# Kernel optimization log

Measured on AMD Instinct MI355X. Metric: run time of the kernel, lower is better.

## Reference

```python
import jax, jax.numpy as jnp
import numpy as np

B, N, C = 16, 2048, 3           # images, proposals/image, classes (incl. background)
K = 100                         # num_detections kept per class
SCORE_THRESH = 0.05
NMS_THRESH = 0.5
MIN_ANGLE = 10.0                # process_box min width (self.min_angle)
WX, WW = 1.0, 1.0               # box_coder reg_weights
NEG = jnp.float32(-1e9)


def setup_inputs() -> dict:
    key = jax.random.key(0)
    k1, k2, k3, k4 = jax.random.split(key, 4)
    class_logit = jax.random.normal(k1, (B, N, C), jnp.float32)
    box_regression = jax.random.normal(k2, (B, N, 2 * C), jnp.float32) * 0.1
    starts = jax.random.uniform(k3, (B, N), dtype=jnp.float32) * 300.0
    widths = jax.random.uniform(k4, (B, N), dtype=jnp.float32) * 50.0 + 12.0
    proposal = jnp.stack([starts, starts + widths], axis=-1)  # [B,N,2] 1-D intervals
    return {"class_logit": class_logit, "box_regression": box_regression,
            "proposal": proposal, "image_shape": 360}


def _decode(delta, prop):
    w = prop[:, 1] - prop[:, 0]
    ctr = prop[:, 0] + 0.5 * w
    dx = delta[:, 0] / WX
    dw = jnp.minimum(delta[:, 1] / WW, 4.0)  # clamp like torchvision
    pc = dx * w + ctr
    pw = jnp.exp(dw) * w
    return jnp.stack([pc - 0.5 * pw, pc + 0.5 * pw], axis=-1)  # [N,2]


def _iou_1d(a, b):
    inter = jnp.maximum(0.0, jnp.minimum(a[:, None, 1], b[None, :, 1])
                        - jnp.maximum(a[:, None, 0], b[None, :, 0]))
    union = (a[:, None, 1] - a[:, None, 0]) + (b[None, :, 1] - b[None, :, 0]) - inter
    return inter / jnp.maximum(union, 1e-8)  # [Na,Nb]


def _infer_one_class(score, delta, prop, image_shape):
    # score [N], delta [N,2], prop [N,2] -> [K,3] (start, end, score); invalid slots score=NEG
    box = _decode(delta, prop)
    lo = jnp.clip(box[:, 0], 0.0, image_shape)
    hi = jnp.clip(box[:, 1], 0.0, image_shape)
    box = jnp.stack([lo, hi], axis=-1)
    valid = ((hi - lo) >= MIN_ANGLE) & (score >= SCORE_THRESH)
    ms = jnp.where(valid, score, NEG)
    order = jnp.argsort(-ms)
    b = box[order]
    s = ms[order]
    sup = jax.lax.stop_gradient(_iou_1d(b, b)) > NMS_THRESH  # [N,N] bool
    idx = jnp.arange(N)

    def body(keep, i):  # greedy NMS in score order
        kill = sup[i] & keep[i] & (idx > i)
        return keep & ~kill, None

    keep0 = s > 0.5 * NEG
    keep, _ = jax.lax.scan(body, keep0, idx)
    ks = jnp.where(keep, s, NEG)
    top_s, top_i = jax.lax.top_k(ks, K)
    top_b = b[top_i]
    return jnp.concatenate([top_b, top_s[:, None]], axis=-1)  # [K,3]


def reference(class_logit, box_regression, proposal, image_shape):
    img = jnp.float32(image_shape)
    scores = jax.nn.softmax(class_logit, axis=-1)[..., 1:]        # [B,N,C-1] fg classes
    deltas = box_regression.reshape(B, N, C, 2)[:, :, 1:]         # [B,N,C-1,2]
    scores = jnp.moveaxis(scores, -1, 1)                          # [B,C-1,N]
    deltas = jnp.moveaxis(deltas, 2, 1)                           # [B,C-1,N,2]
    f = jax.vmap(jax.vmap(_infer_one_class, in_axes=(0, 0, None, None)),
                 in_axes=(0, 0, 0, None))
    return f(scores, deltas, proposal, img)  # [B, C-1, K, 3]
```

## Files before the change

kernel.cpp:

```cpp
#include <hip/hip_runtime.h>
#include <math.h>

#define B_IMG 16
#define N_PROP 2048
#define C_CLS 3
#define K_OUT 100
#define NTHREADS 1024
#define NWAVES (NTHREADS / 64)
#define NBLK64 (N_PROP / 64)
#define NUNITS (B_IMG * N_PROP)

__device__ __forceinline__ unsigned long long shfl_xor_u64(unsigned long long v, int lx) {
    unsigned int lo = (unsigned int)__shfl_xor((int)(unsigned int)(v & 0xffffffffull), lx, 64);
    unsigned int hi = (unsigned int)__shfl_xor((int)(unsigned int)(v >> 32), lx, 64);
    return ((unsigned long long)hi << 32) | (unsigned long long)lo;
}
__device__ __forceinline__ float readlane_f(float v, int l) {
    return __int_as_float(__builtin_amdgcn_readlane(__float_as_int(v), l));
}
__device__ __forceinline__ bool iou_gt_half(float inter, float uni) {
    double b = (double)fmaxf(uni, 1e-8f);
    return (double)inter * 2.0 > b * 0x1.000001p0;
}
__device__ __forceinline__ float parse_imgf(int raw) {
    return (raw > 0 && raw < 1000000) ? (float)raw : __int_as_float(raw);
}

__global__ __launch_bounds__(256)
void decode_kernel(const float* __restrict__ class_logit,
                   const float* __restrict__ box_reg,
                   const float* __restrict__ proposal,
                   const int* __restrict__ image_shape_p,
                   unsigned long long* __restrict__ wskey,
                   float2* __restrict__ wbox)
{
#pragma clang fp contract(off)
    const int t = blockIdx.x * 256 + threadIdx.x;
    const int n = t & (N_PROP - 1);
    const float imgf = parse_imgf(image_shape_p[0]);

    const float* lg = class_logit + (size_t)t * C_CLS;
    float l0 = lg[0], l1 = lg[1], l2 = lg[2];
    float mx = fmaxf(l0, fmaxf(l1, l2));
    float e0 = (float)exp((double)(l0 - mx));
    float e1 = (float)exp((double)(l1 - mx));
    float e2 = (float)exp((double)(l2 - mx));
    float denom = (e0 + e1) + e2;

    const float* pp = proposal + (size_t)t * 2;
    float pA = pp[0], pB = pp[1];
    float w = pB - pA;
    float ctr = pA + 0.5f * w;

    const float* dr = box_reg + (size_t)t * (2 * C_CLS);
    float d1x = dr[2], d1w = dr[3], d2x = dr[4], d2w = dr[5];

#pragma unroll
    for (int c = 0; c < 2; ++c) {
        float score = ((c == 0) ? e1 : e2) / denom;
        float dx = (c == 0) ? d1x : d2x;
        float dw = fminf((c == 0) ? d1w : d2w, 4.0f);
        float tt = dx * w;
        float pc = tt + ctr;
        float pw = (float)exp((double)dw) * w;
        float half = 0.5f * pw;
        float lo = pc - half;
        float hi = pc + half;
        lo = fminf(fmaxf(lo, 0.0f), imgf);
        hi = fminf(fmaxf(hi, 0.0f), imgf);
        bool valid = ((hi - lo) >= 10.0f) && (score >= 0.05f);
        float ms = valid ? score : -1e9f;
        unsigned int u = __float_as_uint(ms);
        unsigned int e = (u & 0x80000000u) ? ~u : (u | 0x80000000u);
        wskey[c * NUNITS + t] = ((unsigned long long)e << 32) |
                                (unsigned long long)(0xFFFFFFFFu - (unsigned int)n);
        wbox[c * NUNITS + t] = make_float2(lo, hi);
    }
}

__global__ __launch_bounds__(NTHREADS)
void roiheads_kernel(const unsigned long long* __restrict__ wskey,
                     const float2* __restrict__ wbox,
                     float* __restrict__ out)
{
#pragma clang fp contract(off)
    __shared__ unsigned long long skey[N_PROP];
    __shared__ float slo[N_PROP], shi[N_PROP];
    __shared__ unsigned char keep[N_PROP];
    __shared__ unsigned short alv[2][N_PROP];
    __shared__ float clo[64], chi[64];
    __shared__ unsigned long long kmask[NBLK64];
    __shared__ int wsum[NWAVES];
    __shared__ int sh_nvalid, sh_ccnt;

    const int tid = threadIdx.x;
    const int lane = tid & 63;
    const int wid = tid >> 6;
    const int img = blockIdx.x >> 1;
    const int cls = blockIdx.x & 1;
    const size_t base = (size_t)cls * NUNITS + (size_t)img * N_PROP;

    if (tid == 0) sh_nvalid = 0;

    const int p0 = (wid << 7) | (lane << 1);
    const int p1 = p0 | 1;

    unsigned long long r0 = wskey[base + p0];
    unsigned long long r1 = wskey[base + p1];

    auto pass_inreg = [&](int k, int j) {
        if (j == 1) {
            bool desc = ((p0 & k) == 0);
            bool sw = desc ? (r0 < r1) : (r0 > r1);
            if (sw) { unsigned long long t = r0; r0 = r1; r1 = t; }
        } else {
            int lx = j >> 1;
            unsigned long long o0 = shfl_xor_u64(r0, lx);
            unsigned long long o1 = shfl_xor_u64(r1, lx);
            bool desc = ((p0 & k) == 0);
            bool lower = ((p0 & j) == 0);
            bool takeMax = (lower == desc);
            r0 = takeMax ? (r0 > o0 ? r0 : o0) : (r0 < o0 ? r0 : o0);
            r1 = takeMax ? (r1 > o1 ? r1 : o1) : (r1 < o1 ? r1 : o1);
        }
    };

    for (int k = 2; k <= 128; k <<= 1)
        for (int j = k >> 1; j >= 1; j >>= 1)
            pass_inreg(k, j);

    for (int k = 256; k <= N_PROP; k <<= 1) {
        skey[p0] = r0; skey[p1] = r1;
        __syncthreads();
        for (int j = k >> 1; j >= 128; j >>= 1) {
            int i = ((tid & ~(j - 1)) << 1) | (tid & (j - 1));
            int part = i | j;
            unsigned long long a = skey[i], b = skey[part];
            bool desc_blk = ((i & k) == 0);
            bool sw = desc_blk ? (a < b) : (a > b);
            if (sw) { skey[i] = b; skey[part] = a; }
            __syncthreads();
        }
        r0 = skey[p0]; r1 = skey[p1];
        for (int j = 64; j >= 1; j >>= 1)
            pass_inreg(k, j);
    }
    skey[p0] = r0; skey[p1] = r1;
    __syncthreads();

    for (int i = tid; i < N_PROP; i += NTHREADS) {
        unsigned long long kk = skey[i];
        unsigned int e = (unsigned int)(kk >> 32);
        unsigned int sb = (e & 0x80000000u) ? (e & 0x7FFFFFFFu) : ~e;
        float s = __uint_as_float(sb);
        unsigned int n = 0xFFFFFFFFu - (unsigned int)(kk & 0xFFFFFFFFull);
        float2 bx = wbox[base + n];
        slo[i] = bx.x;
        shi[i] = bx.y;
        keep[i] = 0;
        bool v = (s > -5e8f);
        unsigned long long mb = __ballot(v);
        if (lane == 0) atomicAdd(&sh_nvalid, __popcll(mb));
        alv[0][i] = (unsigned short)i;
    }
    __syncthreads();

    int na = sh_nvalid;
    int cur = 0;
    int tk = 0;
    const unsigned long long below = (1ull << lane) - 1ull;

    while (na > 0) {
        const int m = (na < 64) ? na : 64;
        if (tid < 64) {
            bool inr = (lane < m);
            unsigned short p = inr ? alv[cur][lane] : (unsigned short)0;
            float blo = inr ? slo[p] : 0.0f;
            float bhi = inr ? shi[p] : 0.0f;
            float bw = bhi - blo;
            unsigned long long A = (m >= 64) ? ~0ull : ((1ull << m) - 1ull);
            unsigned long long kept = 0;
            while (A) {
                int c = __builtin_ctzll(A);
                float cl = readlane_f(blo, c);
                float ch = readlane_f(bhi, c);
                float inter = fmaxf(fminf(bhi, ch) - fmaxf(blo, cl), 0.0f);
                float uni = bw + (ch - cl) - inter;
                bool kill = (lane > c) && iou_gt_half(inter, uni);
                unsigned long long row = __ballot(kill);
                kept |= (1ull << c);
                A &= ~(row | (1ull << c));
            }
            bool alive = inr && ((kept >> lane) & 1ull);
            if (alive) keep[p] = 1;
            int rank = __popcll(kept & below);
            if (alive) { clo[rank] = blo; chi[rank] = bhi; }
            if (lane == 0) sh_ccnt = __popcll(kept);
        }
        __syncthreads();
        const int cnt = sh_ccnt;
        tk += cnt;
        if (tk >= K_OUT) break;

        float klo = 0.0f, khi = 0.0f;
        if (lane < cnt) { klo = clo[lane]; khi = chi[lane]; }
        int base2 = 0;
        for (int start = 64; start < na; start += NTHREADS) {
            int t = start + tid;
            unsigned short q = 0;
            bool surv = false;
            if (t < na) {
                q = alv[cur][t];
                float qlo = slo[q], qhi = shi[q];
                float qw = qhi - qlo;
                bool dead = false;
                for (int r = 0; r < cnt; ++r) {
                    float cl = readlane_f(klo, r);
                    float ch = readlane_f(khi, r);
                    float inter = fmaxf(fminf(qhi, ch) - fmaxf(qlo, cl), 0.0f);
                    float uni = qw + (ch - cl) - inter;
                    dead |= iou_gt_half(inter, uni);
                }
                surv = !dead;
            }
            unsigned long long mb = __ballot(surv);
            if (lane == 0) wsum[wid] = __popcll(mb);
            __syncthreads();
            int off = base2, tot = base2;
            for (int w2 = 0; w2 < NWAVES; ++w2) {
                int c2 = wsum[w2];
                if (w2 < wid) off += c2;
                tot += c2;
            }
            if (surv) alv[cur ^ 1][off + __popcll(mb & below)] = q;
            base2 = tot;
            __syncthreads();
        }
        na = base2;
        cur ^= 1;
    }

    for (int blk = wid; blk < NBLK64; blk += NWAVES) {
        bool kk = keep[blk * 64 + lane] != 0;
        unsigned long long mb = __ballot(kk);
        if (lane == 0) kmask[blk] = mb;
    }
    __syncthreads();
    {
        float* outp = out + (((size_t)img * 2 + cls) * K_OUT) * 3;
        for (int blk = wid; blk < NBLK64; blk += NWAVES) {
            int kc = 0, nc = 0, nk = 0;
            for (int b = 0; b < NBLK64; ++b) {
                int pc = __popcll(kmask[b]);
                nk += pc;
                if (b < blk) { kc += pc; nc += 64 - pc; }
            }
            if (kc >= K_OUT && nk + nc >= K_OUT && nc >= K_OUT) continue;
            int p = blk * 64 + lane;
            unsigned long long mb = kmask[blk];
            bool k = (mb >> lane) & 1ull;
            int rk = kc + __popcll(mb & below);
            int rn = nc + __popcll((~mb) & below);
            if (k) {
                if (rk < K_OUT) {
                    unsigned long long kk2 = skey[p];
                    unsigned int e = (unsigned int)(kk2 >> 32);
                    unsigned int sb = (e & 0x80000000u) ? (e & 0x7FFFFFFFu) : ~e;
                    outp[rk * 3 + 0] = slo[p];
                    outp[rk * 3 + 1] = shi[p];
                    outp[rk * 3 + 2] = __uint_as_float(sb);
                }
            } else {
                int oi = nk + rn;
                if (oi < K_OUT) {
                    outp[oi * 3 + 0] = slo[p];
                    outp[oi * 3 + 1] = shi[p];
                    outp[oi * 3 + 2] = -1e9f;
                }
            }
        }
    }
}

extern "C" void kernel_launch(void* const* d_in, const int* in_sizes, int n_in,
                              void* d_out, int out_size, void* d_ws, size_t ws_size,
                              hipStream_t stream) {
    const float* class_logit = (const float*)d_in[0];
    const float* box_reg     = (const float*)d_in[1];
    const float* prop        = (const float*)d_in[2];
    const int*   image_shape = (const int*)d_in[3];
    float* out = (float*)d_out;

    unsigned long long* wskey = (unsigned long long*)d_ws;
    float2* wbox = (float2*)((char*)d_ws + 2 * NUNITS * sizeof(unsigned long long));

    decode_kernel<<<dim3(NUNITS / 256), dim3(256), 0, stream>>>(
        class_logit, box_reg, prop, image_shape, wskey, wbox);
    roiheads_kernel<<<dim3(B_IMG * 2), dim3(NTHREADS), 0, stream>>>(
        wskey, wbox, out);
}
```

Baseline: 99.51 us.

## Preselect top candidates via histogram and sort only a 512-element subset

Builds a 4096-bin histogram of the top key bits to find a threshold admitting at least 256 top-scoring proposals. It compacts and bitonic-sorts only up to 512 of them, then runs greedy NMS on that subset. If the subset yields fewer than K kept boxes, it falls back to a full 2048-element sort and NMS. The block size drops from 1024 to 256 threads, which reduces sort cost but makes the fallback path and NMS compaction loops slower.

```diff
diff --git a/kernel.cpp b/kernel.cpp
--- a/kernel.cpp
+++ b/kernel.cpp
@@ -5,10 +5,13 @@
 #define N_PROP 2048
 #define C_CLS 3
 #define K_OUT 100
-#define NTHREADS 1024
-#define NWAVES (NTHREADS / 64)
+#define NUNITS (B_IMG * N_PROP)
+
+#define NTH2 256
+#define NW2 (NTH2 / 64)
 #define NBLK64 (N_PROP / 64)
-#define NUNITS (B_IMG * N_PROP)
+#define SORTN 512
+#define TSEL 256
 
 __device__ __forceinline__ unsigned long long shfl_xor_u64(unsigned long long v, int lx) {
     unsigned int lo = (unsigned int)__shfl_xor((int)(unsigned int)(v & 0xffffffffull), lx, 64);
@@ -17,6 +20,9 @@
 }
 __device__ __forceinline__ float readlane_f(float v, int l) {
     return __int_as_float(__builtin_amdgcn_readlane(__float_as_int(v), l));
+}
+__device__ __forceinline__ unsigned int readlane_u32(unsigned int v, int l) {
+    return (unsigned int)__builtin_amdgcn_readlane((int)v, l);
 }
 __device__ __forceinline__ bool iou_gt_half(float inter, float uni) {
     double b = (double)fmaxf(uni, 1e-8f);
@@ -78,20 +84,21 @@
     }
 }
 
-__global__ __launch_bounds__(NTHREADS)
-void roiheads_kernel(const unsigned long long* __restrict__ wskey,
-                     const float2* __restrict__ wbox,
-                     float* __restrict__ out)
+__global__ __launch_bounds__(NTH2)
+void nms_kernel(const unsigned long long* __restrict__ wskey,
+                const float2* __restrict__ wbox,
+                float* __restrict__ out)
 {
 #pragma clang fp contract(off)
     __shared__ unsigned long long skey[N_PROP];
     __shared__ float slo[N_PROP], shi[N_PROP];
     __shared__ unsigned char keep[N_PROP];
     __shared__ unsigned short alv[2][N_PROP];
+    __shared__ unsigned int hist[4096];
     __shared__ float clo[64], chi[64];
     __shared__ unsigned long long kmask[NBLK64];
-    __shared__ int wsum[NWAVES];
-    __shared__ int sh_nvalid, sh_ccnt;
+    __shared__ int wsum[NW2];
+    __shared__ int sh_cnt, sh_nv, sh_ccnt, sh_thr, sh_M;
 
     const int tid = threadIdx.x;
     const int lane = tid & 63;
@@ -99,163 +106,139 @@
     const int img = blockIdx.x >> 1;
     const int cls = blockIdx.x & 1;
     const size_t base = (size_t)cls * NUNITS + (size_t)img * N_PROP;
-
-    if (tid == 0) sh_nvalid = 0;
-
-    const int p0 = (wid << 7) | (lane << 1);
-    const int p1 = p0 | 1;
-
-    unsigned long long r0 = wskey[base + p0];
-    unsigned long long r1 = wskey[base + p1];
-
-    auto pass_inreg = [&](int k, int j) {
-        if (j == 1) {
-            bool desc = ((p0 & k) == 0);
-            bool sw = desc ? (r0 < r1) : (r0 > r1);
-            if (sw) { unsigned long long t = r0; r0 = r1; r1 = t; }
-        } else {
-            int lx = j >> 1;
-            unsigned long long o0 = shfl_xor_u64(r0, lx);
-            unsigned long long o1 = shfl_xor_u64(r1, lx);
-            bool desc = ((p0 & k) == 0);
-            bool lower = ((p0 & j) == 0);
-            bool takeMax = (lower == desc);
-            r0 = takeMax ? (r0 > o0 ? r0 : o0) : (r0 < o0 ? r0 : o0);
-            r1 = takeMax ? (r1 > o1 ? r1 : o1) : (r1 < o1 ? r1 : o1);
-        }
+    const unsigned long long below = (1ull << lane) - 1ull;
+
+    for (int i = tid; i < 4096; i += NTH2) hist[i] = 0;
+    if (tid == 0) { sh_cnt = 0; }
+    __syncthreads();
+
+    unsigned long long k8[8];
+#pragma unroll
+    for (int u = 0; u < 8; ++u) {
+        unsigned long long k = wskey[base + u * NTH2 + tid];
+        k8[u] = k;
+        atomicAdd(&hist[(unsigned int)(k >> 52)], 1u);
+    }
+    __syncthreads();
+
+    if (wid == 0) {
+        unsigned int csum = 0;
+        int b0 = lane * 64;
+        for (int i = 0; i < 64; ++i) csum += hist[b0 + i];
+        unsigned int S = csum;
+        for (int d = 1; d < 64; d <<= 1) {
+            unsigned int t2 = __shfl_down(S, d, 64);
+            if (lane + d < 64) S += t2;
+        }
+        unsigned long long bm = __ballot(S >= (unsigned)TSEL);
+        int lstar = 63 - __clzll((long long)bm);
+        unsigned int Snext = 0;
+        if (lstar < 63) Snext = readlane_u32(S, lstar + 1);
+        if (lane == 0) {
+            unsigned int G = Snext;
+            int b = lstar * 64 + 63;
+            for (; b >= lstar * 64; --b) {
+                G += hist[b];
+                if (G >= (unsigned)TSEL) break;
+            }
+            sh_thr = b; sh_M = (int)G;
+        }
+    }
+    __syncthreads();
+    const unsigned int thr = (unsigned int)sh_thr;
+    const int M = sh_M;
+
+    auto run_nms = [&](int total) -> int {
+#pragma clang fp contract(off)
+        int na = sh_nv;
+        int cur = 0, tk = 0;
+        while (na > 0) {
+            const int m = (na < 64) ? na : 64;
+            if (tid < 64) {
+                bool inr = (lane < m);
+                unsigned short p = inr ? alv[cur][lane] : (unsigned short)0;
+                float blo = inr ? slo[p] : 0.0f;
+                float bhi = inr ? shi[p] : 0.0f;
+                float bw = bhi - blo;
+                unsigned long long A = (m >= 64) ? ~0ull : ((1ull << m) - 1ull);
+                unsigned long long kept = 0;
+                while (A) {
+                    int c = __builtin_ctzll(A);
+                    float cl = readlane_f(blo, c);
+                    float ch = readlane_f(bhi, c);
+                    float inter = fmaxf(fminf(bhi, ch) - fmaxf(blo, cl), 0.0f);
+                    float uni = bw + (ch - cl) - inter;
+                    bool kill = (lane > c) && iou_gt_half(inter, uni);
+                    unsigned long long row = __ballot(kill);
+                    kept |= (1ull << c);
+                    A &= ~(row | (1ull << c));
+                }
+                bool alive = inr && ((kept >> lane) & 1ull);
+                if (alive) keep[p] = 1;
+                int rank = __popcll(kept & below);
+                if (alive) { clo[rank] = blo; chi[rank] = bhi; }
+                if (lane == 0) sh_ccnt = __popcll(kept);
+            }
+            __syncthreads();
+            const int cnt = sh_ccnt;
+            tk += cnt;
+            if (tk >= K_OUT) break;
+
+            float klo = 0.0f, khi = 0.0f;
+            if (lane < cnt) { klo = clo[lane]; khi = chi[lane]; }
+            int base2 = 0;
+            for (int start = 64; start < na; start += NTH2) {
+                int t2 = start + tid;
+                unsigned short q = 0;
+                bool surv = false;
+                if (t2 < na) {
+                    q = alv[cur][t2];
+                    float qlo = slo[q], qhi = shi[q];
+                    float qw = qhi - qlo;
+                    bool dead = false;
+                    for (int r = 0; r < cnt; ++r) {
+                        float cl = readlane_f(klo, r);
+                        float ch = readlane_f(khi, r);
+                        float inter = fmaxf(fminf(qhi, ch) - fmaxf(qlo, cl), 0.0f);
+                        float uni = qw + (ch - cl) - inter;
+                        dead |= iou_gt_half(inter, uni);
+                    }
+                    surv = !dead;
+                }
+                unsigned long long mb = __ballot(surv);
+                if (lane == 0) wsum[wid] = __popcll(mb);
+                __syncthreads();
+                int off = base2, tot = base2;
+                for (int w2 = 0; w2 < NW2; ++w2) {
+                    int c2 = wsum[w2];
+                    if (w2 < wid) off += c2;
+                    tot += c2;
+                }
+                if (surv) alv[cur ^ 1][off + __popcll(mb & below)] = q;
+                base2 = tot;
+                __syncthreads();
+            }
+            na = base2;
+            cur ^= 1;
+        }
+        return tk;
     };
 
-    for (int k = 2; k <= 128; k <<= 1)
-        for (int j = k >> 1; j >= 1; j >>= 1)
-            pass_inreg(k, j);
-
-    for (int k = 256; k <= N_PROP; k <<= 1) {
-        skey[p0] = r0; skey[p1] = r1;
-        __syncthreads();
-        for (int j = k >> 1; j >= 128; j >>= 1) {
-            int i = ((tid & ~(j - 1)) << 1) | (tid & (j - 1));
-            int part = i | j;
-            unsigned long long a = skey[i], b = skey[part];
-            bool desc_blk = ((i & k) == 0);
-            bool sw = desc_blk ? (a < b) : (a > b);
-            if (sw) { skey[i] = b; skey[part] = a; }
-            __syncthreads();
-        }
-        r0 = skey[p0]; r1 = skey[p1];
-        for (int j = 64; j >= 1; j >>= 1)
-            pass_inreg(k, j);
-    }
-    skey[p0] = r0; skey[p1] = r1;
-    __syncthreads();
-
-    for (int i = tid; i < N_PROP; i += NTHREADS) {
-        unsigned long long kk = skey[i];
-        unsigned int e = (unsigned int)(kk >> 32);
-        unsigned int sb = (e & 0x80000000u) ? (e & 0x7FFFFFFFu) : ~e;
-        float s = __uint_as_float(sb);
-        unsigned int n = 0xFFFFFFFFu - (unsigned int)(kk & 0xFFFFFFFFull);
-        float2 bx = wbox[base + n];
-        slo[i] = bx.x;
-        shi[i] = bx.y;
-        keep[i] = 0;
-        bool v = (s > -5e8f);
-        unsigned long long mb = __ballot(v);
-        if (lane == 0) atomicAdd(&sh_nvalid, __popcll(mb));
-        alv[0][i] = (unsigned short)i;
-    }
-    __syncthreads();
-
-    int na = sh_nvalid;
-    int cur = 0;
-    int tk = 0;
-    const unsigned long long below = (1ull << lane) - 1ull;
-
-    while (na > 0) {
-        const int m = (na < 64) ? na : 64;
-        if (tid < 64) {
-            bool inr = (lane < m);
-            unsigned short p = inr ? alv[cur][lane] : (unsigned short)0;
-            float blo = inr ? slo[p] : 0.0f;
-            float bhi = inr ? shi[p] : 0.0f;
-            float bw = bhi - blo;
-            unsigned long long A = (m >= 64) ? ~0ull : ((1ull << m) - 1ull);
-            unsigned long long kept = 0;
-            while (A) {
-                int c = __builtin_ctzll(A);
-                float cl = readlane_f(blo, c);
-                float ch = readlane_f(bhi, c);
-                float inter = fmaxf(fminf(bhi, ch) - fmaxf(blo, cl), 0.0f);
-                float uni = bw + (ch - cl) - inter;
-                bool kill = (lane > c) && iou_gt_half(inter, uni);
-                unsigned long long row = __ballot(kill);
-                kept |= (1ull << c);
-                A &= ~(row | (1ull << c));
-            }
-            bool alive = inr && ((kept >> lane) & 1ull);
-            if (alive) keep[p] = 1;
-            int rank = __popcll(kept & below);
-            if (alive) { clo[rank] = blo; chi[rank] = bhi; }
-            if (lane == 0) sh_ccnt = __popcll(kept);
-        }
-        __syncthreads();
-        const int cnt = sh_ccnt;
-        tk += cnt;
-        if (tk >= K_OUT) break;
-
-        float klo = 0.0f, khi = 0.0f;
-        if (lane < cnt) { klo = clo[lane]; khi = chi[lane]; }
-        int base2 = 0;
-        for (int start = 64; start < na; start += NTHREADS) {
-            int t = start + tid;
-            unsigned short q = 0;
-            bool surv = false;
-            if (t < na) {
-                q = alv[cur][t];
-                float qlo = slo[q], qhi = shi[q];
-                float qw = qhi - qlo;
-                bool dead = false;
-                for (int r = 0; r < cnt; ++r) {
-                    float cl = readlane_f(klo, r);
-                    float ch = readlane_f(khi, r);
-                    float inter = fmaxf(fminf(qhi, ch) - fmaxf(qlo, cl), 0.0f);
-                    float uni = qw + (ch - cl) - inter;
-                    dead |= iou_gt_half(inter, uni);
-                }
-                surv = !dead;
-            }
-            unsigned long long mb = __ballot(surv);
-            if (lane == 0) wsum[wid] = __popcll(mb);
-            __syncthreads();
-            int off = base2, tot = base2;
-            for (int w2 = 0; w2 < NWAVES; ++w2) {
-                int c2 = wsum[w2];
-                if (w2 < wid) off += c2;
-                tot += c2;
-            }
-            if (surv) alv[cur ^ 1][off + __popcll(mb & below)] = q;
-            base2 = tot;
-            __syncthreads();
-        }
-        na = base2;
-        cur ^= 1;
-    }
-
-    for (int blk = wid; blk < NBLK64; blk += NWAVES) {
-        bool kk = keep[blk * 64 + lane] != 0;
-        unsigned long long mb = __ballot(kk);
-        if (lane == 0) kmask[blk] = mb;
-    }
-    __syncthreads();
-    {
+    auto emit = [&](int nblk) {
+        for (int blk = wid; blk < nblk; blk += NW2) {
+            bool kk = keep[blk * 64 + lane] != 0;
+            unsigned long long mb = __ballot(kk);
+            if (lane == 0) kmask[blk] = mb;
+        }
+        __syncthreads();
         float* outp = out + (((size_t)img * 2 + cls) * K_OUT) * 3;
-        for (int blk = wid; blk < NBLK64; blk += NWAVES) {
+        for (int blk = wid; blk < nblk; blk += NW2) {
             int kc = 0, nc = 0, nk = 0;
-            for (int b = 0; b < NBLK64; ++b) {
+            for (int b = 0; b < nblk; ++b) {
                 int pc = __popcll(kmask[b]);
                 nk += pc;
                 if (b < blk) { kc += pc; nc += 64 - pc; }
             }
-            if (kc >= K_OUT && nk + nc >= K_OUT && nc >= K_OUT) continue;
             int p = blk * 64 + lane;
             unsigned long long mb = kmask[blk];
             bool k = (mb >> lane) & 1ull;
@@ -279,6 +262,120 @@
                 }
             }
         }
+    };
+
+    bool done = false;
+    if (M <= SORTN) {
+        int myc = 0;
+#pragma unroll
+        for (int u = 0; u < 8; ++u) myc += ((unsigned int)(k8[u] >> 52) >= thr);
+        int off = atomicAdd(&sh_cnt, myc);
+#pragma unroll
+        for (int u = 0; u < 8; ++u)
+            if ((unsigned int)(k8[u] >> 52) >= thr) skey[off++] = k8[u];
+        for (int i = M + tid; i < SORTN; i += NTH2) skey[i] = 0ull;
+        __syncthreads();
+
+        const int p0 = (wid << 7) | (lane << 1);
+        const int p1 = p0 | 1;
+        unsigned long long r0 = skey[p0], r1 = skey[p1];
+        auto pass_inreg = [&](int k, int j) {
+            if (j == 1) {
+                bool desc = ((p0 & k) == 0);
+                bool sw = desc ? (r0 < r1) : (r0 > r1);
+                if (sw) { unsigned long long t2 = r0; r0 = r1; r1 = t2; }
+            } else {
+                int lx = j >> 1;
+                unsigned long long o0 = shfl_xor_u64(r0, lx);
+                unsigned long long o1 = shfl_xor_u64(r1, lx);
+                bool desc = ((p0 & k) == 0);
+                bool lower = ((p0 & j) == 0);
+                bool takeMax = (lower == desc);
+                r0 = takeMax ? (r0 > o0 ? r0 : o0) : (r0 < o0 ? r0 : o0);
+                r1 = takeMax ? (r1 > o1 ? r1 : o1) : (r1 < o1 ? r1 : o1);
+            }
+        };
+        for (int k = 2; k <= 128; k <<= 1)
+            for (int j = k >> 1; j >= 1; j >>= 1)
+                pass_inreg(k, j);
+        for (int k = 256; k <= SORTN; k <<= 1) {
+            skey[p0] = r0; skey[p1] = r1;
+            __syncthreads();
+            for (int j = k >> 1; j >= 128; j >>= 1) {
+                int i = ((tid & ~(j - 1)) << 1) | (tid & (j - 1));
+                int part = i | j;
+                unsigned long long a = skey[i], b = skey[part];
+                bool desc_blk = ((i & k) == 0);
+                bool sw = desc_blk ? (a < b) : (a > b);
+                if (sw) { skey[i] = b; skey[part] = a; }
+                __syncthreads();
+            }
+            r0 = skey[p0]; r1 = skey[p1];
+            for (int j = 64; j >= 1; j >>= 1)
+                pass_inreg(k, j);
+        }
+        skey[p0] = r0; skey[p1] = r1;
+        if (tid == 0) sh_nv = 0;
+        __syncthreads();
+
+        for (int i = tid; i < SORTN; i += NTH2) {
+            unsigned long long kk = skey[i];
+            unsigned int e = (unsigned int)(kk >> 32);
+            unsigned int sb = (e & 0x80000000u) ? (e & 0x7FFFFFFFu) : ~e;
+            float s = __uint_as_float(sb);
+            bool inw = (i < M);
+            if (inw) {
+                unsigned int n = 0xFFFFFFFFu - (unsigned int)(kk & 0xFFFFFFFFull);
+                float2 bx = wbox[base + n];
+                slo[i] = bx.x; shi[i] = bx.y;
+            } else { slo[i] = 0.0f; shi[i] = 0.0f; }
+            keep[i] = 0;
+            bool v = inw && (s > -5e8f);
+            unsigned long long mb = __ballot(v);
+            if (lane == 0) atomicAdd(&sh_nv, __popcll(mb));
+            alv[0][i] = (unsigned short)i;
+        }
+        __syncthreads();
+
+        int tk = run_nms(SORTN);
+        if (tk >= K_OUT) { emit(SORTN / 64); done = true; }
+    }
+
+    if (!done) {
+        __syncthreads();
+        for (int i = tid; i < N_PROP; i += NTH2) skey[i] = wskey[base + i];
+        if (tid == 0) sh_nv = 0;
+        __syncthreads();
+        for (int k = 2; k <= N_PROP; k <<= 1) {
+            for (int j = k >> 1; j >= 1; j >>= 1) {
+                for (int s = tid; s < N_PROP / 2; s += NTH2) {
+                    int i = ((s & ~(j - 1)) << 1) | (s & (j - 1));
+                    int part = i | j;
+                    unsigned long long a = skey[i], b = skey[part];
+                    bool desc_blk = ((i & k) == 0);
+                    bool sw = desc_blk ? (a < b) : (a > b);
+                    if (sw) { skey[i] = b; skey[part] = a; }
+                }
+                __syncthreads();
+            }
+        }
+        for (int i = tid; i < N_PROP; i += NTH2) {
+            unsigned long long kk = skey[i];
+            unsigned int e = (unsigned int)(kk >> 32);
+            unsigned int sb = (e & 0x80000000u) ? (e & 0x7FFFFFFFu) : ~e;
+            float s = __uint_as_float(sb);
+            unsigned int n = 0xFFFFFFFFu - (unsigned int)(kk & 0xFFFFFFFFull);
+            float2 bx = wbox[base + n];
+            slo[i] = bx.x; shi[i] = bx.y;
+            keep[i] = 0;
+            bool v = (s > -5e8f);
+            unsigned long long mb = __ballot(v);
+            if (lane == 0) atomicAdd(&sh_nv, __popcll(mb));
+            alv[0][i] = (unsigned short)i;
+        }
+        __syncthreads();
+        (void)run_nms(N_PROP);
+        emit(NBLK64);
     }
 }
 
@@ -296,6 +393,5 @@
 
     decode_kernel<<<dim3(NUNITS / 256), dim3(256), 0, stream>>>(
         class_logit, box_reg, prop, image_shape, wskey, wbox);
-    roiheads_kernel<<<dim3(B_IMG * 2), dim3(NTHREADS), 0, stream>>>(
-        wskey, wbox, out);
-}
+    nms_kernel<<<dim3(B_IMG * 2), dim3(NTH2), 0, stream>>>(wskey, wbox, out);
+}
```

After: 159.3 us. +60.1%, slower.

## Build 64x64 suppression matrix across all waves, resolve greedy chain via readlane

Applied to the files above, without the earlier changes.

Replaces the single-wave serial NMS over each 64-candidate chunk with a parallel step. All 16 waves compute rows of a 64x64 IoU suppression bitmask into shared memory, then every wave redundantly resolves the greedy keep chain with scalar readlanes of the bitmask rows. This takes the IoU arithmetic out of the serial dependency chain, at the cost of an extra barrier and redundant chain resolution in every wave.

```diff
diff --git a/kernel.cpp b/kernel.cpp
--- a/kernel.cpp
+++ b/kernel.cpp
@@ -17,6 +17,11 @@
 }
 __device__ __forceinline__ float readlane_f(float v, int l) {
     return __int_as_float(__builtin_amdgcn_readlane(__float_as_int(v), l));
+}
+__device__ __forceinline__ unsigned long long readlane_u64(unsigned long long v, int l) {
+    unsigned int lo = (unsigned int)__builtin_amdgcn_readlane((int)(unsigned int)(v & 0xffffffffull), l);
+    unsigned int hi = (unsigned int)__builtin_amdgcn_readlane((int)(unsigned int)(v >> 32), l);
+    return ((unsigned long long)hi << 32) | (unsigned long long)lo;
 }
 __device__ __forceinline__ bool iou_gt_half(float inter, float uni) {
     double b = (double)fmaxf(uni, 1e-8f);
@@ -89,9 +94,10 @@
     __shared__ unsigned char keep[N_PROP];
     __shared__ unsigned short alv[2][N_PROP];
     __shared__ float clo[64], chi[64];
+    __shared__ unsigned long long sup[64];
     __shared__ unsigned long long kmask[NBLK64];
     __shared__ int wsum[NWAVES];
-    __shared__ int sh_nvalid, sh_ccnt;
+    __shared__ int sh_nvalid;
 
     const int tid = threadIdx.x;
     const int lane = tid & 63;
@@ -172,33 +178,47 @@
 
     while (na > 0) {
         const int m = (na < 64) ? na : 64;
-        if (tid < 64) {
-            bool inr = (lane < m);
-            unsigned short p = inr ? alv[cur][lane] : (unsigned short)0;
-            float blo = inr ? slo[p] : 0.0f;
-            float bhi = inr ? shi[p] : 0.0f;
-            float bw = bhi - blo;
-            unsigned long long A = (m >= 64) ? ~0ull : ((1ull << m) - 1ull);
-            unsigned long long kept = 0;
-            while (A) {
-                int c = __builtin_ctzll(A);
-                float cl = readlane_f(blo, c);
-                float ch = readlane_f(bhi, c);
-                float inter = fmaxf(fminf(bhi, ch) - fmaxf(blo, cl), 0.0f);
-                float uni = bw + (ch - cl) - inter;
-                bool kill = (lane > c) && iou_gt_half(inter, uni);
-                unsigned long long row = __ballot(kill);
-                kept |= (1ull << c);
-                A &= ~(row | (1ull << c));
-            }
-            bool alive = inr && ((kept >> lane) & 1ull);
-            if (alive) keep[p] = 1;
-            int rank = __popcll(kept & below);
-            if (alive) { clo[rank] = blo; chi[rank] = bhi; }
-            if (lane == 0) sh_ccnt = __popcll(kept);
+
+        unsigned short cp = alv[cur][lane];
+        bool cin = (lane < m);
+        float qloc = cin ? slo[cp] : 0.0f;
+        float qhic = cin ? shi[cp] : 0.0f;
+
+#pragma unroll
+        for (int rr4 = 0; rr4 < 4; ++rr4) {
+            int rr = (wid << 2) | rr4;
+            unsigned long long row = 0;
+            if (rr < m) {
+                unsigned short rp = alv[cur][rr];
+                float rlo = slo[rp], rhi = shi[rp];
+                float inter = fmaxf(fminf(rhi, qhic) - fmaxf(rlo, qloc), 0.0f);
+                float uni = (rhi - rlo) + (qhic - qloc) - inter;
+                bool kill = cin && (lane > rr) && iou_gt_half(inter, uni);
+                row = __ballot(kill);
+            }
+            if (lane == 0) sup[rr] = row;
         }
         __syncthreads();
-        const int cnt = sh_ccnt;
+
+        unsigned long long rw = sup[lane];
+        unsigned long long A = (m >= 64) ? ~0ull : ((1ull << m) - 1ull);
+        unsigned long long kept = 0;
+        while (A) {
+            int c = __builtin_ctzll(A);
+            kept |= (1ull << c);
+            A &= ~(readlane_u64(rw, c) | (1ull << c));
+        }
+        const int cnt = __popcll(kept);
+
+        if (wid == 0) {
+            bool alive = cin && ((kept >> lane) & 1ull);
+            if (alive) {
+                keep[cp] = 1;
+                int rank = __popcll(kept & below);
+                clo[rank] = qloc; chi[rank] = qhic;
+            }
+        }
+        __syncthreads();
         tk += cnt;
         if (tk >= K_OUT) break;
 
@@ -206,11 +226,11 @@
         if (lane < cnt) { klo = clo[lane]; khi = chi[lane]; }
         int base2 = 0;
         for (int start = 64; start < na; start += NTHREADS) {
-            int t = start + tid;
+            int t2 = start + tid;
             unsigned short q = 0;
             bool surv = false;
-            if (t < na) {
-                q = alv[cur][t];
+            if (t2 < na) {
+                q = alv[cur][t2];
                 float qlo = slo[q], qhi = shi[q];
                 float qw = qhi - qlo;
                 bool dead = false;
```

New measurement: 97.94 us. No clear change (-1.6%).
